# Kernel optimization log

Hardware: AMD Instinct MI355X
Metric: run time of the kernel (lower is better)

## Reference

```python
import math
import jax, jax.numpy as jnp
import numpy as np

S = 30.0
M = 0.5
COS_M = math.cos(M)
SIN_M = math.sin(M)
THRESHOLD = math.cos(math.pi - M)
MM = math.sin(math.pi - M) * M


def setup_inputs() -> dict:
    key = jax.random.key(0)
    k1, k2, k3 = jax.random.split(key, 3)
    B, D, C = 512, 512, 100000
    return {
        "embeddings": jax.random.normal(k1, (B, D), dtype=jnp.float32),
        "kernel": jax.random.normal(k2, (D, C), dtype=jnp.float32) * 0.01,
        "label": jax.random.randint(k3, (B,), 0, C),
        "t": jnp.zeros((1,), dtype=jnp.float32),
    }


def reference(embeddings, kernel, label, t):
    B = embeddings.shape[0]
    # dual L2 normalization (rows of embeddings, columns of kernel)
    emb = embeddings / jnp.linalg.norm(embeddings, ord=2, axis=1, keepdims=True)
    kn = kernel / jnp.linalg.norm(kernel, ord=2, axis=0, keepdims=True)
    # [B, C] cosine similarity, clamped
    cosine = jnp.clip(emb @ kn, -1.0, 1.0)
    rows = jnp.arange(B)
    target_logit = cosine[rows, label][:, None]  # [B, 1]
    sin_theta = jnp.sqrt(1.0 - target_logit ** 2)
    cos_theta_m = target_logit * COS_M - sin_theta * SIN_M  # cos(theta + m)
    # hard negatives: cosine > cos(theta_y + m)
    mask = cosine > cos_theta_m
    final_target = jnp.where(target_logit > THRESHOLD, cos_theta_m, target_logit - MM)
    # EMA update of t (no-grad in the original)
    t_new = target_logit.mean() * 0.01 + 0.99 * t  # shape (1,)
    # scale hard negatives by (t + cosine), fused predicated write
    scaled = jnp.where(mask, cosine * (t_new[0] + cosine), cosine)
    # scatter target logit back into its column
    out = scaled.at[rows, label].set(final_target[:, 0])
    return out * S
```

## Files before the change

kernel.cpp:

```cpp
#include <hip/hip_runtime.h>

#define CC 100000
#define DD 512

#define S_SCALE 30.0f
#define COS_M_C 0.8775825618903728f
#define SIN_M_C 0.479425538604203f
#define THRESH_C (-0.8775825618903728f)
#define MM_C 0.2397127693021015f

typedef __attribute__((ext_vector_type(8))) short short8;
typedef __attribute__((ext_vector_type(4))) float f32x4;

static __device__ __forceinline__ unsigned short f2bf(float x) {
  unsigned int u = __float_as_uint(x);
  unsigned int r = (u + 0x7fffu + ((u >> 16) & 1u)) >> 16;
  return (unsigned short)r;
}

#define FENCE() __builtin_amdgcn_sched_barrier(0)

__global__ __launch_bounds__(64) void k1_prep(
    const float* __restrict__ emb, const float* __restrict__ kern,
    const int* __restrict__ label, unsigned short* __restrict__ wsA,
    float* __restrict__ ws_target, float* __restrict__ ws_ctm,
    float* __restrict__ ws_ft) {
  const int i = blockIdx.x;
  const int l = threadIdx.x;

  const float4* er = reinterpret_cast<const float4*>(emb + (size_t)i * DD + l * 8);
  float4 v0 = er[0], v1 = er[1];
  float e[8] = {v0.x, v0.y, v0.z, v0.w, v1.x, v1.y, v1.z, v1.w};

  float esq = 0.f;
#pragma unroll
  for (int j = 0; j < 8; ++j) esq += e[j] * e[j];
#pragma unroll
  for (int o = 32; o > 0; o >>= 1) esq += __shfl_xor(esq, o);
  const float inv = rsqrtf(esq);

  const int c = label[i];
  float dot = 0.f, wsq = 0.f;
#pragma unroll
  for (int j = 0; j < 8; ++j) {
    float w = kern[(size_t)(l * 8 + j) * CC + c];
    dot += e[j] * w;
    wsq += w * w;
  }
#pragma unroll
  for (int o = 32; o > 0; o >>= 1) {
    dot += __shfl_xor(dot, o);
    wsq += __shfl_xor(wsq, o);
  }

  unsigned int pk[4];
#pragma unroll
  for (int j = 0; j < 4; ++j) {
    unsigned int lo = f2bf(e[2 * j] * inv);
    unsigned int hi = f2bf(e[2 * j + 1] * inv);
    pk[j] = lo | (hi << 16);
  }
  const int off = (l >> 2) * 32768 + (i >> 6) * 4096 + (((i >> 4) & 3)) * 1024 +
                  ((l & 3) * 16 + (i & 15)) * 16;
  uint4 v; v.x = pk[0]; v.y = pk[1]; v.z = pk[2]; v.w = pk[3];
  *reinterpret_cast<uint4*>(reinterpret_cast<char*>(wsA) + off) = v;

  if (l == 0) {
    float t = dot * rsqrtf(fmaxf(esq * wsq, 1e-30f));
    t = fminf(fmaxf(t, -1.f), 1.f);
    float st = sqrtf(fmaxf(0.f, 1.f - t * t));
    float ctm = t * COS_M_C - st * SIN_M_C;
    ws_target[i] = t;
    ws_ctm[i] = ctm;
    ws_ft[i] = (t > THRESH_C) ? ctm : (t - MM_C);
  }
}

__global__ __launch_bounds__(64) void k2_tnew(const float* __restrict__ ws_target,
                                              const float* __restrict__ t_in,
                                              float* __restrict__ ws_tnew) {
  const int l = threadIdx.x;
  float s = 0.f;
#pragma unroll
  for (int j = 0; j < 8; ++j) s += ws_target[l * 8 + j];
#pragma unroll
  for (int o = 32; o > 0; o >>= 1) s += __shfl_xor(s, o);
  if (l == 0) ws_tnew[0] = 0.01f * (s * (1.0f / 512.0f)) + 0.99f * t_in[0];
}

__global__ __launch_bounds__(256, 4) void k3_gemm(
    const float* __restrict__ kern, const unsigned short* __restrict__ wsA,
    const int* __restrict__ label, const float* __restrict__ ws_ctm,
    const float* __restrict__ ws_ft, const float* __restrict__ ws_tnew,
    float* __restrict__ out) {
  __shared__ __align__(16) char smem[8192 + 4352];
  __shared__ float colsq[64];

  const int t = threadIdx.x;
  const int l = t & 63;
  const int wv = t >> 6;
  const int lr = l & 15;
  const int lg = l >> 4;
  const int nt = blockIdx.x >> 1;
  const int mt = blockIdx.x & 1;
  const int n0 = nt * 64;
  const int bm0 = mt * 256;

  if (t < 64) colsq[t] = 0.f;

  const int bn = l;
  const int gcol = n0 + bn;
  const bool colok = gcol < CC;
  const float* bcol = kern + gcol;

  float sumsq = 0.f;

  f32x4 acc[4][4];
#pragma unroll
  for (int a = 0; a < 4; ++a)
#pragma unroll
    for (int b = 0; b < 4; ++b) acc[a][b] = (f32x4){0.f, 0.f, 0.f, 0.f};

  char* Bb = smem;
  const char* pA =
      reinterpret_cast<const char*>(wsA) + (mt * 4 + wv) * 4096 + l * 16;
  const int swz = ((lg ^ (lr & 3) ^ ((lr >> 2) & 3)) << 4);
  const int wb = bn * 64 + (((wv ^ (bn & 3) ^ ((bn >> 2) & 3))) << 4);

#define BLOAD8(KT, r0, r1, r2, r3, r4, r5, r6, r7)                       \
  {                                                                      \
    if (colok) {                                                         \
      const float* q_ = bcol + (size_t)((KT) * 32 + wv * 8) * CC;        \
      r0 = q_[0];              r1 = q_[(size_t)CC];                      \
      r2 = q_[(size_t)2 * CC]; r3 = q_[(size_t)3 * CC];                  \
      r4 = q_[(size_t)4 * CC]; r5 = q_[(size_t)5 * CC];                  \
      r6 = q_[(size_t)6 * CC]; r7 = q_[(size_t)7 * CC];                  \
    } else {                                                             \
      r0 = r1 = r2 = r3 = r4 = r5 = r6 = r7 = 0.f;                       \
    }                                                                    \
  }

#define BWRITE8(KT, r0, r1, r2, r3, r4, r5, r6, r7)                      \
  {                                                                      \
    sumsq += r0 * r0 + r1 * r1 + r2 * r2 + r3 * r3 + r4 * r4 + r5 * r5 + \
             r6 * r6 + r7 * r7;                                          \
    uint4 pk_;                                                           \
    pk_.x = (unsigned int)f2bf(r0) | ((unsigned int)f2bf(r1) << 16);     \
    pk_.y = (unsigned int)f2bf(r2) | ((unsigned int)f2bf(r3) << 16);     \
    pk_.z = (unsigned int)f2bf(r4) | ((unsigned int)f2bf(r5) << 16);     \
    pk_.w = (unsigned int)f2bf(r6) | ((unsigned int)f2bf(r7) << 16);     \
    *reinterpret_cast<uint4*>(Bb + ((KT)&1) * 4096 + wb) = pk_;          \
  }

  float q0, q1, q2, q3, q4, q5, q6, q7;
  float p0, p1, p2, p3, p4, p5, p6, p7;
  BLOAD8(0, q0, q1, q2, q3, q4, q5, q6, q7);
  FENCE();
  BLOAD8(1, p0, p1, p2, p3, p4, p5, p6, p7);
  FENCE();
  asm volatile("s_waitcnt vmcnt(8)" ::: "memory");
  BWRITE8(0, q0, q1, q2, q3, q4, q5, q6, q7);
  asm volatile("s_waitcnt lgkmcnt(0)" ::: "memory");
  FENCE();
  __builtin_amdgcn_s_barrier();
  FENCE();

  for (int kt = 0; kt < 16; ++kt) {
    const int cur = kt & 1;
    short8 af[4];
#pragma unroll
    for (int mf = 0; mf < 4; ++mf)
      af[mf] = *reinterpret_cast<const short8*>(pA + kt * 32768 + mf * 1024);
    FENCE();
    if (kt < 15) {
      asm volatile("s_waitcnt vmcnt(4)" ::: "memory");
      BWRITE8(kt + 1, p0, p1, p2, p3, p4, p5, p6, p7);
    }
    if (kt < 14) {
      BLOAD8(kt + 2, p0, p1, p2, p3, p4, p5, p6, p7);
    }
    FENCE();
    short8 bfr[4];
#pragma unroll
    for (int nf = 0; nf < 4; ++nf) {
      const int n = nf * 16 + lr;
      bfr[nf] = *reinterpret_cast<const short8*>(Bb + cur * 4096 + n * 64 + swz);
    }
    if (kt < 14) {
      asm volatile("s_waitcnt vmcnt(8)" ::: "memory");
    } else {
      asm volatile("s_waitcnt vmcnt(0)" ::: "memory");
    }
    asm volatile("s_waitcnt lgkmcnt(0)" ::: "memory");
    FENCE();
    __builtin_amdgcn_s_setprio(1);
#pragma unroll
    for (int mf = 0; mf < 4; ++mf)
#pragma unroll
      for (int nf = 0; nf < 4; ++nf)
        acc[mf][nf] = __builtin_amdgcn_mfma_f32_16x16x32_bf16(
            af[mf], bfr[nf], acc[mf][nf], 0, 0, 0);
    __builtin_amdgcn_s_setprio(0);
    FENCE();
    __builtin_amdgcn_s_barrier();
    FENCE();
  }

  atomicAdd(&colsq[bn], sumsq);
  asm volatile("s_waitcnt lgkmcnt(0)" ::: "memory");
  FENCE();
  __builtin_amdgcn_s_barrier();
  FENCE();

  const float tnew = ws_tnew[0];
  float invn[4];
#pragma unroll
  for (int nf = 0; nf < 4; ++nf)
    invn[nf] = rsqrtf(fmaxf(colsq[nf * 16 + lr], 1e-30f));

  float* est = reinterpret_cast<float*>(smem + 8192) + (size_t)wv * 272;
  const int c4 = n0 + lr * 4;
#pragma unroll
  for (int mf = 0; mf < 4; ++mf) {
#pragma unroll
    for (int p = 0; p < 4; ++p) {
      asm volatile("s_waitcnt lgkmcnt(0)" ::: "memory");
      FENCE();
      if (lg == p) {
#pragma unroll
        for (int r = 0; r < 4; ++r)
#pragma unroll
          for (int nf = 0; nf < 4; ++nf)
            est[r * 68 + nf * 16 + lr] = acc[mf][nf][r] * invn[nf];
      }
      asm volatile("s_waitcnt lgkmcnt(0)" ::: "memory");
      FENCE();
      const int m = bm0 + wv * 64 + mf * 16 + p * 4 + lg;
      const float ctm = ws_ctm[m];
      const float ft = ws_ft[m];
      const int lab = label[m];
      float4 vv = *reinterpret_cast<const float4*>(&est[lg * 68 + lr * 4]);
      if (c4 < CC) {
        float ov[4] = {vv.x, vv.y, vv.z, vv.w};
#pragma unroll
        for (int j = 0; j < 4; ++j) {
          float cosv = fminf(fmaxf(ov[j], -1.f), 1.f);
          float val = (cosv > ctm) ? cosv * (tnew + cosv) : cosv;
          if (c4 + j == lab) val = ft;
          ov[j] = val * S_SCALE;
        }
        float4 st4;
        st4.x = ov[0]; st4.y = ov[1]; st4.z = ov[2]; st4.w = ov[3];
        *reinterpret_cast<float4*>(out + (size_t)m * CC + c4) = st4;
      }
    }
  }
#undef BLOAD8
#undef BWRITE8
}

extern "C" void kernel_launch(void* const* d_in, const int* in_sizes, int n_in,
                              void* d_out, int out_size, void* d_ws,
                              size_t ws_size, hipStream_t stream) {
  (void)in_sizes; (void)n_in; (void)out_size; (void)ws_size;
  const float* emb = (const float*)d_in[0];
  const float* kern = (const float*)d_in[1];
  const int* label = (const int*)d_in[2];
  const float* t_in = (const float*)d_in[3];
  float* out = (float*)d_out;

  char* ws = (char*)d_ws;
  unsigned short* wsA = (unsigned short*)ws;
  float* ws_target = (float*)(ws + 524288);
  float* ws_ctm = (float*)(ws + 526336);
  float* ws_ft = (float*)(ws + 528384);
  float* ws_tnew = (float*)(ws + 530432);

  k1_prep<<<512, 64, 0, stream>>>(emb, kern, label, wsA, ws_target, ws_ctm, ws_ft);
  k2_tnew<<<1, 64, 0, stream>>>(ws_target, t_in, ws_tnew);
  const int ntiles = (CC + 63) / 64;
  k3_gemm<<<ntiles * 2, 256, 0, stream>>>(kern, wsA, label, ws_ctm, ws_ft,
                                          ws_tnew, out);
}
```

Before: 159.1 us.

## Shrink GEMM block tile to 128x64 with 2x2 waves and XCD-aware block mapping

Each block of the fused GEMM+epilogue now covers 128 rows instead of 256. The four waves are arranged 2x2 over M and N, so each wave computes a 64x32 subtile with half the accumulators. Blocks are remapped so the four M tiles of a given N tile, and neighbouring N tiles, are grouped per XCD for L2 reuse of the kernel columns. Occupancy is raised to 5 blocks per CU through launch bounds and smaller epilogue shared memory. The tradeoffs are that each kernel column is now loaded and normalized by four blocks instead of two, and the output stores narrow from float4 to float2.

```diff
diff --git a/kernel.cpp b/kernel.cpp
--- a/kernel.cpp
+++ b/kernel.cpp
@@ -2,6 +2,7 @@
 
 #define CC 100000
 #define DD 512
+#define NTT 1563
 
 #define S_SCALE 30.0f
 #define COS_M_C 0.8775825618903728f
@@ -88,23 +89,28 @@
   if (l == 0) ws_tnew[0] = 0.01f * (s * (1.0f / 512.0f)) + 0.99f * t_in[0];
 }
 
-__global__ __launch_bounds__(256, 4) void k3_gemm(
+__global__ __launch_bounds__(256, 5) void k3_gemm(
     const float* __restrict__ kern, const unsigned short* __restrict__ wsA,
     const int* __restrict__ label, const float* __restrict__ ws_ctm,
     const float* __restrict__ ws_ft, const float* __restrict__ ws_tnew,
     float* __restrict__ out) {
-  __shared__ __align__(16) char smem[8192 + 4352];
+  __shared__ __align__(16) char smem[8192 + 2304];
   __shared__ float colsq[64];
 
   const int t = threadIdx.x;
   const int l = t & 63;
   const int wv = t >> 6;
+  const int mw = wv >> 1;
+  const int nh = (wv & 1) * 32;
   const int lr = l & 15;
   const int lg = l >> 4;
-  const int nt = blockIdx.x >> 1;
-  const int mt = blockIdx.x & 1;
+
+  const int xcd = blockIdx.x & 7;
+  const int g = blockIdx.x >> 3;
+  const int mt = g & 3;
+  const int nt = (g >> 2) * 8 + xcd;
+  if (nt >= NTT) return;
   const int n0 = nt * 64;
-  const int bm0 = mt * 256;
 
   if (t < 64) colsq[t] = 0.f;
 
@@ -115,16 +121,15 @@
 
   float sumsq = 0.f;
 
-  f32x4 acc[4][4];
+  f32x4 acc[4][2];
 #pragma unroll
   for (int a = 0; a < 4; ++a)
 #pragma unroll
-    for (int b = 0; b < 4; ++b) acc[a][b] = (f32x4){0.f, 0.f, 0.f, 0.f};
+    for (int b = 0; b < 2; ++b) acc[a][b] = (f32x4){0.f, 0.f, 0.f, 0.f};
 
   char* Bb = smem;
   const char* pA =
-      reinterpret_cast<const char*>(wsA) + (mt * 4 + wv) * 4096 + l * 16;
-  const int swz = ((lg ^ (lr & 3) ^ ((lr >> 2) & 3)) << 4);
+      reinterpret_cast<const char*>(wsA) + (mt * 2 + mw) * 4096 + l * 16;
   const int wb = bn * 64 + (((wv ^ (bn & 3) ^ ((bn >> 2) & 3))) << 4);
 
 #define BLOAD8(KT, r0, r1, r2, r3, r4, r5, r6, r7)                       \
@@ -180,11 +185,12 @@
       BLOAD8(kt + 2, p0, p1, p2, p3, p4, p5, p6, p7);
     }
     FENCE();
-    short8 bfr[4];
-#pragma unroll
-    for (int nf = 0; nf < 4; ++nf) {
-      const int n = nf * 16 + lr;
-      bfr[nf] = *reinterpret_cast<const short8*>(Bb + cur * 4096 + n * 64 + swz);
+    short8 bfr[2];
+#pragma unroll
+    for (int nf = 0; nf < 2; ++nf) {
+      const int n = nh + nf * 16 + lr;
+      bfr[nf] = *reinterpret_cast<const short8*>(
+          Bb + cur * 4096 + n * 64 + (((lg ^ (n & 3) ^ ((n >> 2) & 3))) << 4));
     }
     if (kt < 14) {
       asm volatile("s_waitcnt vmcnt(8)" ::: "memory");
@@ -197,7 +203,7 @@
 #pragma unroll
     for (int mf = 0; mf < 4; ++mf)
 #pragma unroll
-      for (int nf = 0; nf < 4; ++nf)
+      for (int nf = 0; nf < 2; ++nf)
         acc[mf][nf] = __builtin_amdgcn_mfma_f32_16x16x32_bf16(
             af[mf], bfr[nf], acc[mf][nf], 0, 0, 0);
     __builtin_amdgcn_s_setprio(0);
@@ -213,13 +219,13 @@
   FENCE();
 
   const float tnew = ws_tnew[0];
-  float invn[4];
-#pragma unroll
-  for (int nf = 0; nf < 4; ++nf)
-    invn[nf] = rsqrtf(fmaxf(colsq[nf * 16 + lr], 1e-30f));
-
-  float* est = reinterpret_cast<float*>(smem + 8192) + (size_t)wv * 272;
-  const int c4 = n0 + lr * 4;
+  float invn[2];
+#pragma unroll
+  for (int nf = 0; nf < 2; ++nf)
+    invn[nf] = rsqrtf(fmaxf(colsq[nh + nf * 16 + lr], 1e-30f));
+
+  float* est = reinterpret_cast<float*>(smem + 8192) + (size_t)wv * 144;
+  const int c2 = n0 + nh + lr * 2;
 #pragma unroll
   for (int mf = 0; mf < 4; ++mf) {
 #pragma unroll
@@ -230,28 +236,28 @@
 #pragma unroll
         for (int r = 0; r < 4; ++r)
 #pragma unroll
-          for (int nf = 0; nf < 4; ++nf)
-            est[r * 68 + nf * 16 + lr] = acc[mf][nf][r] * invn[nf];
+          for (int nf = 0; nf < 2; ++nf)
+            est[r * 36 + nf * 16 + lr] = acc[mf][nf][r] * invn[nf];
       }
       asm volatile("s_waitcnt lgkmcnt(0)" ::: "memory");
       FENCE();
-      const int m = bm0 + wv * 64 + mf * 16 + p * 4 + lg;
+      const int m = mt * 128 + mw * 64 + mf * 16 + p * 4 + lg;
       const float ctm = ws_ctm[m];
       const float ft = ws_ft[m];
       const int lab = label[m];
-      float4 vv = *reinterpret_cast<const float4*>(&est[lg * 68 + lr * 4]);
-      if (c4 < CC) {
-        float ov[4] = {vv.x, vv.y, vv.z, vv.w};
-#pragma unroll
-        for (int j = 0; j < 4; ++j) {
-          float cosv = fminf(fmaxf(ov[j], -1.f), 1.f);
+      float2 vv = *reinterpret_cast<const float2*>(&est[lg * 36 + lr * 2]);
+      if (c2 < CC) {
+        float ov[2] = {vv.x, vv.y};
+#pragma unroll
+        for (int jj = 0; jj < 2; ++jj) {
+          float cosv = fminf(fmaxf(ov[jj], -1.f), 1.f);
           float val = (cosv > ctm) ? cosv * (tnew + cosv) : cosv;
-          if (c4 + j == lab) val = ft;
-          ov[j] = val * S_SCALE;
+          if (c2 + jj == lab) val = ft;
+          ov[jj] = val * S_SCALE;
         }
-        float4 st4;
-        st4.x = ov[0]; st4.y = ov[1]; st4.z = ov[2]; st4.w = ov[3];
-        *reinterpret_cast<float4*>(out + (size_t)m * CC + c4) = st4;
+        float2 st2;
+        st2.x = ov[0]; st2.y = ov[1];
+        *reinterpret_cast<float2*>(out + (size_t)m * CC + c2) = st2;
       }
     }
   }
@@ -278,7 +284,6 @@
 
   k1_prep<<<512, 64, 0, stream>>>(emb, kern, label, wsA, ws_target, ws_ctm, ws_ft);
   k2_tnew<<<1, 64, 0, stream>>>(ws_target, t_in, ws_tnew);
-  const int ntiles = (CC + 63) / 64;
-  k3_gemm<<<ntiles * 2, 256, 0, stream>>>(kern, wsA, label, ws_ctm, ws_ft,
-                                          ws_tnew, out);
-}
+  k3_gemm<<<196 * 32, 256, 0, stream>>>(kern, wsA, label, ws_ctm, ws_ft,
+                                        ws_tnew, out);
+}
```

New measurement: 188.8 us. 18.6% more time.

## Cover all 512 rows per block so each kernel column tile is loaded once

Applied to the files above, without the earlier changes.

The GEMM block grows from 256 to 512 threads (8 waves) and now covers all 512 batch rows for a 64-column tile, instead of splitting the rows across two blocks. Each fp32 kernel column is therefore read from global memory and converted to bf16 only once rather than twice, which halves the dominant kernel-matrix traffic. The K step per iteration doubles to 64 with a wider LDS tile and an XOR swizzle, and B-fragment reads are interleaved with the MFMA groups. In exchange the block uses more LDS and registers (8 A fragments), there are half as many blocks, and each barrier now synchronises 8 waves.

```diff
diff --git a/kernel.cpp b/kernel.cpp
--- a/kernel.cpp
+++ b/kernel.cpp
@@ -88,12 +88,12 @@
   if (l == 0) ws_tnew[0] = 0.01f * (s * (1.0f / 512.0f)) + 0.99f * t_in[0];
 }
 
-__global__ __launch_bounds__(256, 4) void k3_gemm(
+__global__ __launch_bounds__(512, 4) void k3_gemm(
     const float* __restrict__ kern, const unsigned short* __restrict__ wsA,
     const int* __restrict__ label, const float* __restrict__ ws_ctm,
     const float* __restrict__ ws_ft, const float* __restrict__ ws_tnew,
     float* __restrict__ out) {
-  __shared__ __align__(16) char smem[8192 + 4352];
+  __shared__ __align__(16) char smem[16384 + 8704];
   __shared__ float colsq[64];
 
   const int t = threadIdx.x;
@@ -101,10 +101,7 @@
   const int wv = t >> 6;
   const int lr = l & 15;
   const int lg = l >> 4;
-  const int nt = blockIdx.x >> 1;
-  const int mt = blockIdx.x & 1;
-  const int n0 = nt * 64;
-  const int bm0 = mt * 256;
+  const int n0 = blockIdx.x * 64;
 
   if (t < 64) colsq[t] = 0.f;
 
@@ -122,15 +119,13 @@
     for (int b = 0; b < 4; ++b) acc[a][b] = (f32x4){0.f, 0.f, 0.f, 0.f};
 
   char* Bb = smem;
-  const char* pA =
-      reinterpret_cast<const char*>(wsA) + (mt * 4 + wv) * 4096 + l * 16;
-  const int swz = ((lg ^ (lr & 3) ^ ((lr >> 2) & 3)) << 4);
-  const int wb = bn * 64 + (((wv ^ (bn & 3) ^ ((bn >> 2) & 3))) << 4);
-
-#define BLOAD8(KT, r0, r1, r2, r3, r4, r5, r6, r7)                       \
+  const char* pA = reinterpret_cast<const char*>(wsA) + wv * 4096 + l * 16;
+  const int wb = bn * 128 + ((wv ^ (bn & 7)) << 4);
+
+#define BLOAD8(G, r0, r1, r2, r3, r4, r5, r6, r7)                        \
   {                                                                      \
     if (colok) {                                                         \
-      const float* q_ = bcol + (size_t)((KT) * 32 + wv * 8) * CC;        \
+      const float* q_ = bcol + (size_t)((G) * 64 + wv * 8) * CC;         \
       r0 = q_[0];              r1 = q_[(size_t)CC];                      \
       r2 = q_[(size_t)2 * CC]; r3 = q_[(size_t)3 * CC];                  \
       r4 = q_[(size_t)4 * CC]; r5 = q_[(size_t)5 * CC];                  \
@@ -140,7 +135,7 @@
     }                                                                    \
   }
 
-#define BWRITE8(KT, r0, r1, r2, r3, r4, r5, r6, r7)                      \
+#define BWRITE8(G, r0, r1, r2, r3, r4, r5, r6, r7)                       \
   {                                                                      \
     sumsq += r0 * r0 + r1 * r1 + r2 * r2 + r3 * r3 + r4 * r4 + r5 * r5 + \
              r6 * r6 + r7 * r7;                                          \
@@ -149,8 +144,13 @@
     pk_.y = (unsigned int)f2bf(r2) | ((unsigned int)f2bf(r3) << 16);     \
     pk_.z = (unsigned int)f2bf(r4) | ((unsigned int)f2bf(r5) << 16);     \
     pk_.w = (unsigned int)f2bf(r6) | ((unsigned int)f2bf(r7) << 16);     \
-    *reinterpret_cast<uint4*>(Bb + ((KT)&1) * 4096 + wb) = pk_;          \
-  }
+    *reinterpret_cast<uint4*>(Bb + ((G)&1) * 8192 + wb) = pk_;           \
+  }
+
+#define BREAD(NF, H)                                                      \
+  (*reinterpret_cast<const short8*>(                                      \
+      Bb + cur * 8192 + (NF * 16 + lr) * 128 +                            \
+      ((((H) * 4 + lg) ^ ((NF * 16 + lr) & 7)) << 4)))
 
   float q0, q1, q2, q3, q4, q5, q6, q7;
   float p0, p1, p2, p3, p4, p5, p6, p7;
@@ -165,28 +165,26 @@
   __builtin_amdgcn_s_barrier();
   FENCE();
 
-  for (int kt = 0; kt < 16; ++kt) {
-    const int cur = kt & 1;
-    short8 af[4];
-#pragma unroll
-    for (int mf = 0; mf < 4; ++mf)
-      af[mf] = *reinterpret_cast<const short8*>(pA + kt * 32768 + mf * 1024);
-    FENCE();
-    if (kt < 15) {
-      asm volatile("s_waitcnt vmcnt(4)" ::: "memory");
-      BWRITE8(kt + 1, p0, p1, p2, p3, p4, p5, p6, p7);
-    }
-    if (kt < 14) {
-      BLOAD8(kt + 2, p0, p1, p2, p3, p4, p5, p6, p7);
-    }
-    FENCE();
-    short8 bfr[4];
-#pragma unroll
-    for (int nf = 0; nf < 4; ++nf) {
-      const int n = nf * 16 + lr;
-      bfr[nf] = *reinterpret_cast<const short8*>(Bb + cur * 4096 + n * 64 + swz);
-    }
-    if (kt < 14) {
+  for (int g = 0; g < 8; ++g) {
+    const int cur = g & 1;
+    short8 af[8];
+#pragma unroll
+    for (int mf = 0; mf < 4; ++mf) {
+      af[mf] = *reinterpret_cast<const short8*>(pA + g * 65536 + mf * 1024);
+      af[4 + mf] =
+          *reinterpret_cast<const short8*>(pA + g * 65536 + 32768 + mf * 1024);
+    }
+    FENCE();
+    asm volatile("s_waitcnt vmcnt(8)" ::: "memory");
+    if (g < 7) {
+      BWRITE8(g + 1, p0, p1, p2, p3, p4, p5, p6, p7);
+    }
+    if (g < 6) {
+      BLOAD8(g + 2, p0, p1, p2, p3, p4, p5, p6, p7);
+    }
+    FENCE();
+    short8 b0 = BREAD(0, 0), b1 = BREAD(1, 0);
+    if (g < 6) {
       asm volatile("s_waitcnt vmcnt(8)" ::: "memory");
     } else {
       asm volatile("s_waitcnt vmcnt(0)" ::: "memory");
@@ -195,11 +193,42 @@
     FENCE();
     __builtin_amdgcn_s_setprio(1);
 #pragma unroll
-    for (int mf = 0; mf < 4; ++mf)
-#pragma unroll
-      for (int nf = 0; nf < 4; ++nf)
-        acc[mf][nf] = __builtin_amdgcn_mfma_f32_16x16x32_bf16(
-            af[mf], bfr[nf], acc[mf][nf], 0, 0, 0);
+    for (int mf = 0; mf < 4; ++mf) {
+      acc[mf][0] = __builtin_amdgcn_mfma_f32_16x16x32_bf16(af[mf], b0,
+                                                           acc[mf][0], 0, 0, 0);
+      acc[mf][1] = __builtin_amdgcn_mfma_f32_16x16x32_bf16(af[mf], b1,
+                                                           acc[mf][1], 0, 0, 0);
+    }
+    b0 = BREAD(2, 0); b1 = BREAD(3, 0);
+    asm volatile("s_waitcnt lgkmcnt(0)" ::: "memory");
+    FENCE();
+#pragma unroll
+    for (int mf = 0; mf < 4; ++mf) {
+      acc[mf][2] = __builtin_amdgcn_mfma_f32_16x16x32_bf16(af[mf], b0,
+                                                           acc[mf][2], 0, 0, 0);
+      acc[mf][3] = __builtin_amdgcn_mfma_f32_16x16x32_bf16(af[mf], b1,
+                                                           acc[mf][3], 0, 0, 0);
+    }
+    b0 = BREAD(0, 1); b1 = BREAD(1, 1);
+    asm volatile("s_waitcnt lgkmcnt(0)" ::: "memory");
+    FENCE();
+#pragma unroll
+    for (int mf = 0; mf < 4; ++mf) {
+      acc[mf][0] = __builtin_amdgcn_mfma_f32_16x16x32_bf16(af[4 + mf], b0,
+                                                           acc[mf][0], 0, 0, 0);
+      acc[mf][1] = __builtin_amdgcn_mfma_f32_16x16x32_bf16(af[4 + mf], b1,
+                                                           acc[mf][1], 0, 0, 0);
+    }
+    b0 = BREAD(2, 1); b1 = BREAD(3, 1);
+    asm volatile("s_waitcnt lgkmcnt(0)" ::: "memory");
+    FENCE();
+#pragma unroll
+    for (int mf = 0; mf < 4; ++mf) {
+      acc[mf][2] = __builtin_amdgcn_mfma_f32_16x16x32_bf16(af[4 + mf], b0,
+                                                           acc[mf][2], 0, 0, 0);
+      acc[mf][3] = __builtin_amdgcn_mfma_f32_16x16x32_bf16(af[4 + mf], b1,
+                                                           acc[mf][3], 0, 0, 0);
+    }
     __builtin_amdgcn_s_setprio(0);
     FENCE();
     __builtin_amdgcn_s_barrier();
@@ -218,7 +247,7 @@
   for (int nf = 0; nf < 4; ++nf)
     invn[nf] = rsqrtf(fmaxf(colsq[nf * 16 + lr], 1e-30f));
 
-  float* est = reinterpret_cast<float*>(smem + 8192) + (size_t)wv * 272;
+  float* est = reinterpret_cast<float*>(smem + 16384) + (size_t)wv * 272;
   const int c4 = n0 + lr * 4;
 #pragma unroll
   for (int mf = 0; mf < 4; ++mf) {
@@ -235,7 +264,7 @@
       }
       asm volatile("s_waitcnt lgkmcnt(0)" ::: "memory");
       FENCE();
-      const int m = bm0 + wv * 64 + mf * 16 + p * 4 + lg;
+      const int m = wv * 64 + mf * 16 + p * 4 + lg;
       const float ctm = ws_ctm[m];
       const float ft = ws_ft[m];
       const int lab = label[m];
@@ -243,11 +272,11 @@
       if (c4 < CC) {
         float ov[4] = {vv.x, vv.y, vv.z, vv.w};
 #pragma unroll
-        for (int j = 0; j < 4; ++j) {
-          float cosv = fminf(fmaxf(ov[j], -1.f), 1.f);
+        for (int jj = 0; jj < 4; ++jj) {
+          float cosv = fminf(fmaxf(ov[jj], -1.f), 1.f);
           float val = (cosv > ctm) ? cosv * (tnew + cosv) : cosv;
-          if (c4 + j == lab) val = ft;
-          ov[j] = val * S_SCALE;
+          if (c4 + jj == lab) val = ft;
+          ov[jj] = val * S_SCALE;
         }
         float4 st4;
         st4.x = ov[0]; st4.y = ov[1]; st4.z = ov[2]; st4.w = ov[3];
@@ -257,6 +286,7 @@
   }
 #undef BLOAD8
 #undef BWRITE8
+#undef BREAD
 }
 
 extern "C" void kernel_launch(void* const* d_in, const int* in_sizes, int n_in,
@@ -278,7 +308,6 @@
 
   k1_prep<<<512, 64, 0, stream>>>(emb, kern, label, wsA, ws_target, ws_ctm, ws_ft);
   k2_tnew<<<1, 64, 0, stream>>>(ws_target, t_in, ws_tnew);
-  const int ntiles = (CC + 63) / 64;
-  k3_gemm<<<ntiles * 2, 256, 0, stream>>>(kern, wsA, label, ws_ctm, ws_ft,
-                                          ws_tnew, out);
-}
+  k3_gemm<<<(CC + 63) / 64, 512, 0, stream>>>(kern, wsA, label, ws_ctm, ws_ft,
+                                              ws_tnew, out);
+}
```

Result: slower. 385.8 us (+142.4%).
